# Performance work log

Hardware: AMD Instinct MI355X
Metric: run time of the kernel (lower is better)

## Reference

```python
import jax, jax.numpy as jnp
import numpy as np

EPS = 1e-5

def _ln(x, w, b):
    mu = jnp.mean(x, axis=-1, keepdims=True)
    var = jnp.var(x, axis=-1, keepdims=True)
    return (x - mu) * jax.lax.rsqrt(var + EPS) * w + b

def setup_inputs() -> dict:
    key = jax.random.key(0)
    ks = jax.random.split(key, 12)
    B, N, CZ, CH = 1, 384, 128, 128
    z = jax.random.normal(ks[0], (B, N, N, CZ), dtype=jnp.float32)
    mask = jnp.ones((B, N, N), dtype=jnp.float32)
    s_z = 1.0 / np.sqrt(CZ)
    s_h = 1.0 / np.sqrt(CH)
    return {
        "z": z,
        "mask": mask,
        "ln_in_w": jnp.ones((CZ,), jnp.float32),
        "ln_in_b": jnp.zeros((CZ,), jnp.float32),
        "w_a_g": jax.random.normal(ks[1], (CZ, CH), jnp.float32) * s_z,
        "b_a_g": jnp.ones((CH,), jnp.float32),
        "w_a_p": jax.random.normal(ks[2], (CZ, CH), jnp.float32) * s_z,
        "b_a_p": jnp.zeros((CH,), jnp.float32),
        "w_b_g": jax.random.normal(ks[3], (CZ, CH), jnp.float32) * s_z,
        "b_b_g": jnp.ones((CH,), jnp.float32),
        "w_b_p": jax.random.normal(ks[4], (CZ, CH), jnp.float32) * s_z,
        "b_b_p": jnp.zeros((CH,), jnp.float32),
        "ln_out_w": jnp.ones((CH,), jnp.float32),
        "ln_out_b": jnp.zeros((CH,), jnp.float32),
        "w_z": jax.random.normal(ks[5], (CH, CZ), jnp.float32) * s_h,
        "b_z": jnp.zeros((CZ,), jnp.float32),
        "w_g": jax.random.normal(ks[6], (CZ, CZ), jnp.float32) * s_z,
        "b_g": jnp.ones((CZ,), jnp.float32),
    }

def reference(z, mask, ln_in_w, ln_in_b, w_a_g, b_a_g, w_a_p, b_a_p,
              w_b_g, b_b_g, w_b_p, b_b_p, ln_out_w, ln_out_b,
              w_z, b_z, w_g, b_g):
    m = mask[..., None]                                   # [B,N,N,1]
    zn = _ln(z, ln_in_w, ln_in_b)                         # [B,N,N,Cz]
    a = m * jax.nn.sigmoid(zn @ w_a_g + b_a_g) * (zn @ w_a_p + b_a_p)
    b = m * jax.nn.sigmoid(zn @ w_b_g + b_b_g) * (zn @ w_b_p + b_b_p)
    # outgoing: p[b,i,j,c] = sum_k a[b,i,k,c] * b[b,j,k,c]
    x = jnp.einsum('bikc,bjkc->bijc', a, b)
    x = _ln(x, ln_out_w, ln_out_b)
    x = (x @ w_z + b_z) * jax.nn.sigmoid(zn @ w_g + b_g)
    return x
```

## Files before the change

kernel.cpp:

```cpp
#include <hip/hip_runtime.h>
#include <hip/hip_bf16.h>

#define NN 384
#define NP (NN*NN)
#define CC 128

typedef __attribute__((ext_vector_type(8))) short bf16x8;
typedef __attribute__((ext_vector_type(4))) float f32x4;
typedef __attribute__((ext_vector_type(8))) unsigned short u16x8;
typedef __attribute__((ext_vector_type(4))) unsigned short u16x4;

#define SW16(row, col) ((col) ^ (((row)&15)<<3))
#define SW8(row, col)  ((col) ^ (((row)&7)<<3))

__device__ __forceinline__ unsigned short f2bf(float f){
  unsigned int u = __float_as_uint(f);
  u += 0x7FFFu + ((u >> 16) & 1u);
  return (unsigned short)(u >> 16);
}
__device__ __forceinline__ float bf2f(unsigned short h){
  return __uint_as_float(((unsigned int)h) << 16);
}
__device__ __forceinline__ float sigm(float x){ return 1.f / (1.f + __expf(-x)); }

__global__ __launch_bounds__(256) void k0(const float* __restrict__ w0, const float* __restrict__ w1,
                                          const float* __restrict__ w2, const float* __restrict__ w3,
                                          const float* __restrict__ w4, const float* __restrict__ w5,
                                          unsigned short* __restrict__ Wt)
{
  __shared__ unsigned short t[CC*CC];
  const float* W = blockIdx.x==0?w0: blockIdx.x==1?w1: blockIdx.x==2?w2:
                   blockIdx.x==3?w3: blockIdx.x==4?w4: w5;
  unsigned short* o = Wt + blockIdx.x*CC*CC;
  for (int i = threadIdx.x; i < CC*CC; i += 256){
    int k = i >> 7, n = i & 127;
    t[n*CC + SW16(n, k)] = f2bf(W[i]);
  }
  __syncthreads();
  for (int i = threadIdx.x; i < CC*16; i += 256){
    int n = i >> 4, g = i & 15;
    *(u16x8*)&o[n*CC + g*8] = *(const u16x8*)&t[n*CC + SW16(n, g*8)];
  }
}

__global__ __launch_bounds__(256) void k1(
    const float* __restrict__ z, const float* __restrict__ mask,
    const float* __restrict__ lnw, const float* __restrict__ lnb,
    const float* __restrict__ bag, const float* __restrict__ bap,
    const float* __restrict__ bbg, const float* __restrict__ bbp,
    const float* __restrict__ bgt,
    const unsigned short* __restrict__ Wt,
    unsigned short* __restrict__ At, unsigned short* __restrict__ Bt,
    unsigned short* __restrict__ G)
{
  __shared__ unsigned short zn[CC*CC];
  const int tid = threadIdx.x, wave = tid>>6, lane = tid&63;
  const int l16 = lane&15, lg = lane>>4;
  const int posbase = blockIdx.x*128;

  {
    const int lh = lane&31, hh = lane>>5;
    const float4 lw4 = *(const float4*)&lnw[4*lh];
    const float4 lb4 = *(const float4*)&lnb[4*lh];
    for (int it = 0; it < 16; ++it){
      int pl = wave*32 + it*2 + hh;
      float4 v = *(const float4*)&z[(size_t)(posbase+pl)*CC + 4*lh];
      float s = v.x+v.y+v.z+v.w;
      float q = v.x*v.x+v.y*v.y+v.z*v.z+v.w*v.w;
      #pragma unroll
      for (int off = 16; off; off >>= 1){ s += __shfl_xor(s, off); q += __shfl_xor(q, off); }
      float mean = s*(1.f/128.f);
      float rstd = rsqrtf(q*(1.f/128.f) - mean*mean + 1e-5f);
      u16x4 o;
      o[0] = f2bf((v.x-mean)*rstd*lw4.x + lb4.x);
      o[1] = f2bf((v.y-mean)*rstd*lw4.y + lb4.y);
      o[2] = f2bf((v.z-mean)*rstd*lw4.z + lb4.z);
      o[3] = f2bf((v.w-mean)*rstd*lw4.w + lb4.w);
      *(u16x4*)&zn[pl*CC + SW16(pl, 4*lh)] = o;
    }
  }
  __syncthreads();

  #pragma unroll 1
  for (int pr = 0; pr < 2; ++pr){
    const unsigned short* Wg = Wt + (pr*2+0)*CC*CC;
    const unsigned short* Wp = Wt + (pr*2+1)*CC*CC;
    const float* Bg_ = pr ? bbg : bag;
    const float* Bp_ = pr ? bbp : bap;
    unsigned short* dst = pr ? Bt : At;
    float4 bg4[2], bp4[2];
    #pragma unroll
    for (int ma = 0; ma < 2; ++ma){
      int cb = wave*32 + ma*16 + lg*4;
      bg4[ma] = *(const float4*)&Bg_[cb];
      bp4[ma] = *(const float4*)&Bp_[cb];
    }
    #pragma unroll 1
    for (int half = 0; half < 2; ++half){
      f32x4 ag[2][4] = {}; f32x4 ap[2][4] = {};
      #pragma unroll
      for (int kc = 0; kc < 4; ++kc){
        const int kb = kc*32 + lg*8;
        bf16x8 bz[4], wgf[2], wpf[2];
        #pragma unroll
        for (int nb = 0; nb < 4; ++nb){
          int pos = half*64 + nb*16 + l16;
          bz[nb] = *(const bf16x8*)&zn[pos*CC + SW16(pos, kb)];
        }
        #pragma unroll
        for (int ma = 0; ma < 2; ++ma){
          int c = wave*32 + ma*16 + l16;
          wgf[ma] = *(const bf16x8*)&Wg[c*CC + kb];
          wpf[ma] = *(const bf16x8*)&Wp[c*CC + kb];
        }
        #pragma unroll
        for (int ma = 0; ma < 2; ++ma)
          #pragma unroll
          for (int nb = 0; nb < 4; ++nb){
            ag[ma][nb] = __builtin_amdgcn_mfma_f32_16x16x32_bf16(wgf[ma], bz[nb], ag[ma][nb], 0,0,0);
            ap[ma][nb] = __builtin_amdgcn_mfma_f32_16x16x32_bf16(wpf[ma], bz[nb], ap[ma][nb], 0,0,0);
          }
      }
      #pragma unroll
      for (int nb = 0; nb < 4; ++nb){
        int pos = posbase + half*64 + nb*16 + l16;
        float m = mask[pos];
        #pragma unroll
        for (int ma = 0; ma < 2; ++ma){
          int cb = wave*32 + ma*16 + lg*4;
          #pragma unroll
          for (int r = 0; r < 4; ++r){
            float bgv = r==0?bg4[ma].x : r==1?bg4[ma].y : r==2?bg4[ma].z : bg4[ma].w;
            float bpv = r==0?bp4[ma].x : r==1?bp4[ma].y : r==2?bp4[ma].z : bp4[ma].w;
            float v = m * sigm(ag[ma][nb][r] + bgv) * (ap[ma][nb][r] + bpv);
            dst[(size_t)(cb + r)*NP + pos] = f2bf(v);
          }
        }
      }
    }
  }

  {
    const unsigned short* Wgt = Wt + 4*CC*CC;
    f32x4 acc[2][8] = {};
    #pragma unroll
    for (int kc = 0; kc < 4; ++kc){
      const int kb = kc*32 + lg*8;
      bf16x8 az[2], wf[8];
      #pragma unroll
      for (int ma = 0; ma < 2; ++ma){
        int pos = wave*32 + ma*16 + l16;
        az[ma] = *(const bf16x8*)&zn[pos*CC + SW16(pos, kb)];
      }
      #pragma unroll
      for (int nr = 0; nr < 8; ++nr)
        wf[nr] = *(const bf16x8*)&Wgt[(nr*16+l16)*CC + kb];
      #pragma unroll
      for (int ma = 0; ma < 2; ++ma)
        #pragma unroll
        for (int nr = 0; nr < 8; ++nr)
          acc[ma][nr] = __builtin_amdgcn_mfma_f32_16x16x32_bf16(az[ma], wf[nr], acc[ma][nr], 0,0,0);
    }
    #pragma unroll
    for (int nr = 0; nr < 8; ++nr){
      int c = nr*16 + l16;
      float bv = bgt[c];
      #pragma unroll
      for (int ma = 0; ma < 2; ++ma)
        #pragma unroll
        for (int r = 0; r < 4; ++r){
          int pos = posbase + wave*32 + ma*16 + lg*4 + r;
          G[(size_t)pos*CC + c] = f2bf(sigm(acc[ma][nr][r] + bv));
        }
    }
  }
}

__global__ __launch_bounds__(256) void k2(const unsigned short* __restrict__ At,
                                          const unsigned short* __restrict__ Bt,
                                          unsigned short* __restrict__ Xt)
{
  __shared__ unsigned short As[128*64];
  __shared__ unsigned short Bs[128*64];
  const int c  = blockIdx.y;
  const int ti = blockIdx.x / 3, tj = blockIdx.x % 3;
  const int tid = threadIdx.x, wave = tid >> 6, lane = tid & 63;
  const int l16 = lane & 15, lg = lane >> 4;
  const unsigned short* Ag = At + (size_t)c*NP + (size_t)(ti*128)*NN;
  const unsigned short* Bg = Bt + (size_t)c*NP + (size_t)(tj*128)*NN;
  f32x4 acc[2][8] = {};
  for (int k0 = 0; k0 < NN; k0 += 64){
    __syncthreads();
    #pragma unroll
    for (int it = 0; it < 4; ++it){
      int i = tid + it*256;
      int row = i >> 3, g = i & 7;
      u16x8 va = *(const u16x8*)&Ag[(size_t)row*NN + k0 + g*8];
      u16x8 vb = *(const u16x8*)&Bg[(size_t)row*NN + k0 + g*8];
      *(u16x8*)&As[row*64 + SW8(row, g*8)] = va;
      *(u16x8*)&Bs[row*64 + SW8(row, g*8)] = vb;
    }
    __syncthreads();
    #pragma unroll
    for (int kc = 0; kc < 2; ++kc){
      const int kb = kc*32 + lg*8;
      bf16x8 af[2], bfr[8];
      #pragma unroll
      for (int ma = 0; ma < 2; ++ma){
        int row = wave*32 + ma*16 + l16;
        af[ma] = *(const bf16x8*)&As[row*64 + SW8(row, kb)];
      }
      #pragma unroll
      for (int nr = 0; nr < 8; ++nr){
        int row = nr*16 + l16;
        bfr[nr] = *(const bf16x8*)&Bs[row*64 + SW8(row, kb)];
      }
      #pragma unroll
      for (int ma = 0; ma < 2; ++ma)
        #pragma unroll
        for (int nr = 0; nr < 8; ++nr)
          acc[ma][nr] = __builtin_amdgcn_mfma_f32_16x16x32_bf16(af[ma], bfr[nr], acc[ma][nr], 0,0,0);
    }
  }
  size_t base = (size_t)c*NP + (size_t)(ti*128)*NN + tj*128;
  #pragma unroll
  for (int ma = 0; ma < 2; ++ma)
    #pragma unroll
    for (int nr = 0; nr < 8; ++nr)
      #pragma unroll
      for (int r = 0; r < 4; ++r){
        int row = wave*32 + ma*16 + lg*4 + r;
        int col = nr*16 + l16;
        Xt[base + (size_t)row*NN + col] = f2bf(acc[ma][nr][r]);
      }
}

__global__ __launch_bounds__(256) void k3(const unsigned short* __restrict__ Xt,
                                          const unsigned short* __restrict__ G,
                                          const float* __restrict__ lnw, const float* __restrict__ lnb,
                                          const unsigned short* __restrict__ Wzt, const float* __restrict__ bz,
                                          float* __restrict__ out)
{
  __shared__ unsigned short xc[CC*CC];
  __shared__ unsigned short yt[CC*CC];
  __shared__ float mu[CC], rs[CC];
  const int tid = threadIdx.x, wave = tid>>6, lane = tid&63;
  const int l16 = lane&15, lg = lane>>4;
  const int posbase = blockIdx.x*128;

  #pragma unroll
  for (int it = 0; it < 8; ++it){
    int i = tid + it*256;
    int cc = i >> 4, g = i & 15;
    u16x8 v = *(const u16x8*)&Xt[(size_t)cc*NP + posbase + g*8];
    *(u16x8*)&xc[cc*CC + SW16(cc, g*8)] = v;
  }
  __syncthreads();

  {
    const int lh = lane&31, hh = lane>>5;
    f32x4 s4 = {0,0,0,0}, q4 = {0,0,0,0};
    for (int ci = 0; ci < 64; ++ci){
      int cc = hh*64 + ci;
      u16x4 v = *(const u16x4*)&xc[cc*CC + SW16(cc, 4*lh)];
      #pragma unroll
      for (int j = 0; j < 4; ++j){
        float f = bf2f(v[j]);
        s4[j] += f; q4[j] += f*f;
      }
    }
    #pragma unroll
    for (int j = 0; j < 4; ++j){ s4[j] += __shfl_xor(s4[j], 32); q4[j] += __shfl_xor(q4[j], 32); }
    if (hh == 0){
      f32x4 m4, r4;
      #pragma unroll
      for (int j = 0; j < 4; ++j){
        float mean = s4[j]*(1.f/128.f);
        m4[j] = mean;
        r4[j] = rsqrtf(q4[j]*(1.f/128.f) - mean*mean + 1e-5f);
      }
      *(f32x4*)&mu[4*lh] = m4;
      *(f32x4*)&rs[4*lh] = r4;
    }
  }
  __syncthreads();

  #pragma unroll
  for (int it = 0; it < 8; ++it){
    int i = tid + it*256;
    int cc = i & 127, g = i >> 7;
    u16x8 v = *(const u16x8*)&xc[cc*CC + SW16(cc, g*8)];
    float lw = lnw[cc], lb = lnb[cc];
    #pragma unroll
    for (int j = 0; j < 8; ++j){
      int pos = g*8 + j;
      float f = (bf2f(v[j]) - mu[pos]) * rs[pos] * lw + lb;
      yt[pos*CC + SW16(pos, cc)] = f2bf(f);
    }
  }
  __syncthreads();

  f32x4 acc[2][8] = {};
  #pragma unroll
  for (int kc = 0; kc < 4; ++kc){
    const int kb = kc*32 + lg*8;
    bf16x8 af[2], wf[8];
    #pragma unroll
    for (int ma = 0; ma < 2; ++ma){
      int pos = wave*32 + ma*16 + l16;
      af[ma] = *(const bf16x8*)&yt[pos*CC + SW16(pos, kb)];
    }
    #pragma unroll
    for (int nr = 0; nr < 8; ++nr)
      wf[nr] = *(const bf16x8*)&Wzt[(nr*16+l16)*CC + kb];
    #pragma unroll
    for (int ma = 0; ma < 2; ++ma)
      #pragma unroll
      for (int nr = 0; nr < 8; ++nr)
        acc[ma][nr] = __builtin_amdgcn_mfma_f32_16x16x32_bf16(af[ma], wf[nr], acc[ma][nr], 0,0,0);
  }
  #pragma unroll
  for (int nr = 0; nr < 8; ++nr){
    int cch = nr*16 + l16;
    float bzv = bz[cch];
    #pragma unroll
    for (int ma = 0; ma < 2; ++ma)
      #pragma unroll
      for (int r = 0; r < 4; ++r){
        int pos = posbase + wave*32 + ma*16 + lg*4 + r;
        size_t o = (size_t)pos*CC + cch;
        out[o] = (acc[ma][nr][r] + bzv) * bf2f(G[o]);
      }
  }
}

extern "C" void kernel_launch(void* const* d_in, const int* in_sizes, int n_in,
                              void* d_out, int out_size, void* d_ws, size_t ws_size,
                              hipStream_t stream)
{
  const float* z    = (const float*)d_in[0];
  const float* mask = (const float*)d_in[1];
  const float* lniw = (const float*)d_in[2];
  const float* lnib = (const float*)d_in[3];
  const float* wag  = (const float*)d_in[4];
  const float* bag  = (const float*)d_in[5];
  const float* wap  = (const float*)d_in[6];
  const float* bap  = (const float*)d_in[7];
  const float* wbg  = (const float*)d_in[8];
  const float* bbg  = (const float*)d_in[9];
  const float* wbp  = (const float*)d_in[10];
  const float* bbp  = (const float*)d_in[11];
  const float* lnow = (const float*)d_in[12];
  const float* lnob = (const float*)d_in[13];
  const float* wz   = (const float*)d_in[14];
  const float* bz   = (const float*)d_in[15];
  const float* wg   = (const float*)d_in[16];
  const float* bg   = (const float*)d_in[17];
  float* out = (float*)d_out;

  unsigned short* Wt = (unsigned short*)d_ws;
  unsigned short* At = Wt + 6*CC*CC;
  unsigned short* Bt = At + (size_t)CC*NP;
  unsigned short* G  = Bt + (size_t)CC*NP;
  unsigned short* Xt = G  + (size_t)CC*NP;

  k0<<<6, 256, 0, stream>>>(wag, wap, wbg, wbp, wg, wz, Wt);
  k1<<<NP/128, 256, 0, stream>>>(z, mask, lniw, lnib, bag, bap, bbg, bbp, bg, Wt, At, Bt, G);
  k2<<<dim3(9, CC), 256, 0, stream>>>(At, Bt, Xt);
  k3<<<NP/128, 256, 0, stream>>>(Xt, G, lnow, lnob, Wt + 5*CC*CC, bz, out);
}
```

Before: 400.7 us.

## Split input projection kernel and fold output LayerNorm into projection epilogue

Splits the fused input-LN plus projection kernel into an LN kernel that writes normalized bf16 z to workspace and a projection kernel gridded over 64-row tiles and three projection types (a, b, gate). The tiles are loaded into LDS via global_load_lds. This gives more parallel blocks and lower register and LDS pressure, at the cost of an extra round trip of normalized z through global memory. The output LayerNorm is folded algebraically: the weight is pre-scaled by ln_out_w, and a per-channel weight sum and adjusted bias are precomputed. The projection therefore consumes the raw x tile, applied as rstd*acc - rstd*mean*wsum + b', which removes the normalized intermediate buffer and a pass in k3. Reading A fragments as transposed scalar LDS loads may add LDS instruction cost.

```diff
diff --git a/kernel.cpp b/kernel.cpp
--- a/kernel.cpp
+++ b/kernel.cpp
@@ -13,6 +13,12 @@
 #define SW16(row, col) ((col) ^ (((row)&15)<<3))
 #define SW8(row, col)  ((col) ^ (((row)&7)<<3))
 
+typedef const __attribute__((address_space(1))) unsigned int GLu32;
+typedef __attribute__((address_space(3))) unsigned int LDu32;
+__device__ __forceinline__ void gload_lds16(const void* g, void* l){
+  __builtin_amdgcn_global_load_lds((GLu32*)g, (LDu32*)l, 16, 0, 0);
+}
+
 __device__ __forceinline__ unsigned short f2bf(float f){
   unsigned int u = __float_as_uint(f);
   u += 0x7FFFu + ((u >> 16) & 1u);
@@ -26,15 +32,37 @@
 __global__ __launch_bounds__(256) void k0(const float* __restrict__ w0, const float* __restrict__ w1,
                                           const float* __restrict__ w2, const float* __restrict__ w3,
                                           const float* __restrict__ w4, const float* __restrict__ w5,
-                                          unsigned short* __restrict__ Wt)
-{
+                                          const float* __restrict__ lnow, const float* __restrict__ lnob,
+                                          const float* __restrict__ bz,
+                                          unsigned short* __restrict__ Wt,
+                                          float* __restrict__ wsum, float* __restrict__ bzp)
+{
+  if (blockIdx.x == 6){
+    __shared__ float p1[256], p2[256];
+    int c = threadIdx.x & 127, half = threadIdx.x >> 7;
+    float s1 = 0.f, s2 = 0.f;
+    #pragma unroll 8
+    for (int k = half*64; k < half*64 + 64; ++k){
+      float w = w5[k*CC + c];
+      s1 += lnow[k]*w; s2 += lnob[k]*w;
+    }
+    p1[threadIdx.x] = s1; p2[threadIdx.x] = s2;
+    __syncthreads();
+    if (half == 0){
+      wsum[c] = s1 + p1[128 + c];
+      bzp[c]  = bz[c] + s2 + p2[128 + c];
+    }
+    return;
+  }
   __shared__ unsigned short t[CC*CC];
   const float* W = blockIdx.x==0?w0: blockIdx.x==1?w1: blockIdx.x==2?w2:
                    blockIdx.x==3?w3: blockIdx.x==4?w4: w5;
+  const bool scale = (blockIdx.x == 5);
   unsigned short* o = Wt + blockIdx.x*CC*CC;
   for (int i = threadIdx.x; i < CC*CC; i += 256){
     int k = i >> 7, n = i & 127;
-    t[n*CC + SW16(n, k)] = f2bf(W[i]);
+    float f = W[i] * (scale ? lnow[k] : 1.0f);
+    t[n*CC + SW16(n, k)] = f2bf(f);
   }
   __syncthreads();
   for (int i = threadIdx.x; i < CC*16; i += 256){
@@ -43,135 +71,133 @@
   }
 }
 
-__global__ __launch_bounds__(256) void k1(
-    const float* __restrict__ z, const float* __restrict__ mask,
+__global__ __launch_bounds__(256) void k1a(const float* __restrict__ z,
     const float* __restrict__ lnw, const float* __restrict__ lnb,
+    unsigned short* __restrict__ zng)
+{
+  const int wave = threadIdx.x>>6, lane = threadIdx.x&63;
+  const int lh = lane&31, hh = lane>>5;
+  const float4 lw4 = *(const float4*)&lnw[4*lh];
+  const float4 lb4 = *(const float4*)&lnb[4*lh];
+  const int rowbase = blockIdx.x*128 + wave*32;
+  for (int it = 0; it < 16; ++it){
+    int pos = rowbase + it*2 + hh;
+    float4 v = *(const float4*)&z[(size_t)pos*CC + 4*lh];
+    float s = v.x+v.y+v.z+v.w;
+    float q = v.x*v.x+v.y*v.y+v.z*v.z+v.w*v.w;
+    #pragma unroll
+    for (int off = 16; off; off >>= 1){ s += __shfl_xor(s, off); q += __shfl_xor(q, off); }
+    float mean = s*(1.f/128.f);
+    float rstd = rsqrtf(q*(1.f/128.f) - mean*mean + 1e-5f);
+    u16x4 o;
+    o[0] = f2bf((v.x-mean)*rstd*lw4.x + lb4.x);
+    o[1] = f2bf((v.y-mean)*rstd*lw4.y + lb4.y);
+    o[2] = f2bf((v.z-mean)*rstd*lw4.z + lb4.z);
+    o[3] = f2bf((v.w-mean)*rstd*lw4.w + lb4.w);
+    *(u16x4*)&zng[(size_t)pos*CC + ((4*lh) ^ ((pos&15)<<3))] = o;
+  }
+}
+
+__global__ __launch_bounds__(256,3) void k1b(
+    const unsigned short* __restrict__ zng, const float* __restrict__ mask,
     const float* __restrict__ bag, const float* __restrict__ bap,
     const float* __restrict__ bbg, const float* __restrict__ bbp,
-    const float* __restrict__ bgt,
-    const unsigned short* __restrict__ Wt,
+    const float* __restrict__ bgt, const unsigned short* __restrict__ Wt,
     unsigned short* __restrict__ At, unsigned short* __restrict__ Bt,
     unsigned short* __restrict__ G)
 {
-  __shared__ unsigned short zn[CC*CC];
+  __shared__ unsigned short zn[64*CC];
   const int tid = threadIdx.x, wave = tid>>6, lane = tid&63;
   const int l16 = lane&15, lg = lane>>4;
-  const int posbase = blockIdx.x*128;
+  const int type = blockIdx.y;
+  const int tb = blockIdx.x*64;
 
   {
-    const int lh = lane&31, hh = lane>>5;
-    const float4 lw4 = *(const float4*)&lnw[4*lh];
-    const float4 lb4 = *(const float4*)&lnb[4*lh];
-    for (int it = 0; it < 16; ++it){
-      int pl = wave*32 + it*2 + hh;
-      float4 v = *(const float4*)&z[(size_t)(posbase+pl)*CC + 4*lh];
-      float s = v.x+v.y+v.z+v.w;
-      float q = v.x*v.x+v.y*v.y+v.z*v.z+v.w*v.w;
-      #pragma unroll
-      for (int off = 16; off; off >>= 1){ s += __shfl_xor(s, off); q += __shfl_xor(q, off); }
-      float mean = s*(1.f/128.f);
-      float rstd = rsqrtf(q*(1.f/128.f) - mean*mean + 1e-5f);
-      u16x4 o;
-      o[0] = f2bf((v.x-mean)*rstd*lw4.x + lb4.x);
-      o[1] = f2bf((v.y-mean)*rstd*lw4.y + lb4.y);
-      o[2] = f2bf((v.z-mean)*rstd*lw4.z + lb4.z);
-      o[3] = f2bf((v.w-mean)*rstd*lw4.w + lb4.w);
-      *(u16x4*)&zn[pl*CC + SW16(pl, 4*lh)] = o;
-    }
-  }
-  __syncthreads();
-
-  #pragma unroll 1
-  for (int pr = 0; pr < 2; ++pr){
-    const unsigned short* Wg = Wt + (pr*2+0)*CC*CC;
-    const unsigned short* Wp = Wt + (pr*2+1)*CC*CC;
-    const float* Bg_ = pr ? bbg : bag;
-    const float* Bp_ = pr ? bbp : bap;
-    unsigned short* dst = pr ? Bt : At;
-    float4 bg4[2], bp4[2];
+    const char* src = (const char*)(zng + (size_t)tb*CC);
+    #pragma unroll
+    for (int it = 0; it < 4; ++it){
+      int off = (wave*4 + it)*1024;
+      gload_lds16(src + off + lane*16, (char*)zn + off);
+    }
+  }
+  __syncthreads();
+
+  if (type < 2){
+    const unsigned short* Wg = Wt + (type*2+0)*CC*CC;
+    const unsigned short* Wp = Wt + (type*2+1)*CC*CC;
+    f32x4 ag[2][4] = {}, ap[2][4] = {};
+    #pragma unroll
+    for (int kc = 0; kc < 4; ++kc){
+      const int kb = kc*32 + lg*8;
+      bf16x8 bz[4], wgf[2], wpf[2];
+      #pragma unroll
+      for (int nb = 0; nb < 4; ++nb){
+        int pl = nb*16 + l16;
+        bz[nb] = *(const bf16x8*)&zn[pl*CC + (kb ^ (l16<<3))];
+      }
+      #pragma unroll
+      for (int ma = 0; ma < 2; ++ma){
+        int c = wave*32 + ma*16 + l16;
+        wgf[ma] = *(const bf16x8*)&Wg[c*CC + kb];
+        wpf[ma] = *(const bf16x8*)&Wp[c*CC + kb];
+      }
+      #pragma unroll
+      for (int ma = 0; ma < 2; ++ma)
+        #pragma unroll
+        for (int nb = 0; nb < 4; ++nb){
+          ag[ma][nb] = __builtin_amdgcn_mfma_f32_16x16x32_bf16(wgf[ma], bz[nb], ag[ma][nb], 0,0,0);
+          ap[ma][nb] = __builtin_amdgcn_mfma_f32_16x16x32_bf16(wpf[ma], bz[nb], ap[ma][nb], 0,0,0);
+        }
+    }
+    const float* Bg_ = type ? bbg : bag;
+    const float* Bp_ = type ? bbp : bap;
+    unsigned short* dst = type ? Bt : At;
+    f32x4 bg4[2], bp4[2];
     #pragma unroll
     for (int ma = 0; ma < 2; ++ma){
       int cb = wave*32 + ma*16 + lg*4;
-      bg4[ma] = *(const float4*)&Bg_[cb];
-      bp4[ma] = *(const float4*)&Bp_[cb];
-    }
-    #pragma unroll 1
-    for (int half = 0; half < 2; ++half){
-      f32x4 ag[2][4] = {}; f32x4 ap[2][4] = {};
-      #pragma unroll
-      for (int kc = 0; kc < 4; ++kc){
-        const int kb = kc*32 + lg*8;
-        bf16x8 bz[4], wgf[2], wpf[2];
+      bg4[ma] = *(const f32x4*)&Bg_[cb];
+      bp4[ma] = *(const f32x4*)&Bp_[cb];
+    }
+    #pragma unroll
+    for (int nb = 0; nb < 4; ++nb){
+      int pos = tb + nb*16 + l16;
+      float m = mask[pos];
+      #pragma unroll
+      for (int ma = 0; ma < 2; ++ma){
+        int cb = wave*32 + ma*16 + lg*4;
         #pragma unroll
-        for (int nb = 0; nb < 4; ++nb){
-          int pos = half*64 + nb*16 + l16;
-          bz[nb] = *(const bf16x8*)&zn[pos*CC + SW16(pos, kb)];
+        for (int r = 0; r < 4; ++r){
+          float v = m * sigm(ag[ma][nb][r] + bg4[ma][r]) * (ap[ma][nb][r] + bp4[ma][r]);
+          dst[(size_t)(cb + r)*NP + pos] = f2bf(v);
         }
-        #pragma unroll
-        for (int ma = 0; ma < 2; ++ma){
-          int c = wave*32 + ma*16 + l16;
-          wgf[ma] = *(const bf16x8*)&Wg[c*CC + kb];
-          wpf[ma] = *(const bf16x8*)&Wp[c*CC + kb];
-        }
-        #pragma unroll
-        for (int ma = 0; ma < 2; ++ma)
-          #pragma unroll
-          for (int nb = 0; nb < 4; ++nb){
-            ag[ma][nb] = __builtin_amdgcn_mfma_f32_16x16x32_bf16(wgf[ma], bz[nb], ag[ma][nb], 0,0,0);
-            ap[ma][nb] = __builtin_amdgcn_mfma_f32_16x16x32_bf16(wpf[ma], bz[nb], ap[ma][nb], 0,0,0);
-          }
-      }
-      #pragma unroll
-      for (int nb = 0; nb < 4; ++nb){
-        int pos = posbase + half*64 + nb*16 + l16;
-        float m = mask[pos];
-        #pragma unroll
-        for (int ma = 0; ma < 2; ++ma){
-          int cb = wave*32 + ma*16 + lg*4;
-          #pragma unroll
-          for (int r = 0; r < 4; ++r){
-            float bgv = r==0?bg4[ma].x : r==1?bg4[ma].y : r==2?bg4[ma].z : bg4[ma].w;
-            float bpv = r==0?bp4[ma].x : r==1?bp4[ma].y : r==2?bp4[ma].z : bp4[ma].w;
-            float v = m * sigm(ag[ma][nb][r] + bgv) * (ap[ma][nb][r] + bpv);
-            dst[(size_t)(cb + r)*NP + pos] = f2bf(v);
-          }
-        }
-      }
-    }
-  }
-
-  {
+      }
+    }
+  } else {
     const unsigned short* Wgt = Wt + 4*CC*CC;
-    f32x4 acc[2][8] = {};
+    f32x4 acc[8] = {};
     #pragma unroll
     for (int kc = 0; kc < 4; ++kc){
       const int kb = kc*32 + lg*8;
-      bf16x8 az[2], wf[8];
-      #pragma unroll
-      for (int ma = 0; ma < 2; ++ma){
-        int pos = wave*32 + ma*16 + l16;
-        az[ma] = *(const bf16x8*)&zn[pos*CC + SW16(pos, kb)];
-      }
+      int pl = wave*16 + l16;
+      bf16x8 az = *(const bf16x8*)&zn[pl*CC + (kb ^ (l16<<3))];
+      bf16x8 wf[8];
       #pragma unroll
       for (int nr = 0; nr < 8; ++nr)
         wf[nr] = *(const bf16x8*)&Wgt[(nr*16+l16)*CC + kb];
       #pragma unroll
-      for (int ma = 0; ma < 2; ++ma)
-        #pragma unroll
-        for (int nr = 0; nr < 8; ++nr)
-          acc[ma][nr] = __builtin_amdgcn_mfma_f32_16x16x32_bf16(az[ma], wf[nr], acc[ma][nr], 0,0,0);
+      for (int nr = 0; nr < 8; ++nr)
+        acc[nr] = __builtin_amdgcn_mfma_f32_16x16x32_bf16(az, wf[nr], acc[nr], 0,0,0);
     }
     #pragma unroll
     for (int nr = 0; nr < 8; ++nr){
       int c = nr*16 + l16;
       float bv = bgt[c];
       #pragma unroll
-      for (int ma = 0; ma < 2; ++ma)
-        #pragma unroll
-        for (int r = 0; r < 4; ++r){
-          int pos = posbase + wave*32 + ma*16 + lg*4 + r;
-          G[(size_t)pos*CC + c] = f2bf(sigm(acc[ma][nr][r] + bv));
-        }
+      for (int r = 0; r < 4; ++r){
+        int pos = tb + wave*16 + lg*4 + r;
+        G[(size_t)pos*CC + c] = f2bf(sigm(acc[nr][r] + bv));
+      }
     }
   }
 }
@@ -236,21 +262,20 @@
 }
 
 __global__ __launch_bounds__(256) void k3(const unsigned short* __restrict__ Xt,
-                                          const unsigned short* __restrict__ G,
-                                          const float* __restrict__ lnw, const float* __restrict__ lnb,
-                                          const unsigned short* __restrict__ Wzt, const float* __restrict__ bz,
-                                          float* __restrict__ out)
+    const unsigned short* __restrict__ G,
+    const unsigned short* __restrict__ Wzt, const float* __restrict__ wsum,
+    const float* __restrict__ bzp, float* __restrict__ out)
 {
   __shared__ unsigned short xc[CC*CC];
-  __shared__ unsigned short yt[CC*CC];
-  __shared__ float mu[CC], rs[CC];
+  __shared__ float sredS[8*CC], sredQ[8*CC];
+  __shared__ float rsl[CC], rml[CC];
   const int tid = threadIdx.x, wave = tid>>6, lane = tid&63;
   const int l16 = lane&15, lg = lane>>4;
   const int posbase = blockIdx.x*128;
 
   #pragma unroll
   for (int it = 0; it < 8; ++it){
-    int i = tid + it*256;
+    int i = it*256 + tid;
     int cc = i >> 4, g = i & 15;
     u16x8 v = *(const u16x8*)&Xt[(size_t)cc*NP + posbase + g*8];
     *(u16x8*)&xc[cc*CC + SW16(cc, g*8)] = v;
@@ -258,45 +283,27 @@
   __syncthreads();
 
   {
-    const int lh = lane&31, hh = lane>>5;
+    const int lh = tid & 31;
+    const int qq = tid >> 5;
     f32x4 s4 = {0,0,0,0}, q4 = {0,0,0,0};
-    for (int ci = 0; ci < 64; ++ci){
-      int cc = hh*64 + ci;
-      u16x4 v = *(const u16x4*)&xc[cc*CC + SW16(cc, 4*lh)];
-      #pragma unroll
-      for (int j = 0; j < 4; ++j){
-        float f = bf2f(v[j]);
-        s4[j] += f; q4[j] += f*f;
-      }
-    }
-    #pragma unroll
-    for (int j = 0; j < 4; ++j){ s4[j] += __shfl_xor(s4[j], 32); q4[j] += __shfl_xor(q4[j], 32); }
-    if (hh == 0){
-      f32x4 m4, r4;
-      #pragma unroll
-      for (int j = 0; j < 4; ++j){
-        float mean = s4[j]*(1.f/128.f);
-        m4[j] = mean;
-        r4[j] = rsqrtf(q4[j]*(1.f/128.f) - mean*mean + 1e-5f);
-      }
-      *(f32x4*)&mu[4*lh] = m4;
-      *(f32x4*)&rs[4*lh] = r4;
-    }
-  }
-  __syncthreads();
-
-  #pragma unroll
-  for (int it = 0; it < 8; ++it){
-    int i = tid + it*256;
-    int cc = i & 127, g = i >> 7;
-    u16x8 v = *(const u16x8*)&xc[cc*CC + SW16(cc, g*8)];
-    float lw = lnw[cc], lb = lnb[cc];
-    #pragma unroll
-    for (int j = 0; j < 8; ++j){
-      int pos = g*8 + j;
-      float f = (bf2f(v[j]) - mu[pos]) * rs[pos] * lw + lb;
-      yt[pos*CC + SW16(pos, cc)] = f2bf(f);
-    }
+    #pragma unroll
+    for (int ci = 0; ci < 16; ++ci){
+      int cc = qq*16 + ci;
+      u16x4 v = *(const u16x4*)&xc[cc*CC + ((4*lh) ^ ((cc&15)<<3))];
+      #pragma unroll
+      for (int j = 0; j < 4; ++j){ float f = bf2f(v[j]); s4[j] += f; q4[j] += f*f; }
+    }
+    *(f32x4*)&sredS[qq*CC + 4*lh] = s4;
+    *(f32x4*)&sredQ[qq*CC + 4*lh] = q4;
+  }
+  __syncthreads();
+  if (tid < 128){
+    float s = 0.f, q = 0.f;
+    #pragma unroll
+    for (int qq = 0; qq < 8; ++qq){ s += sredS[qq*CC + tid]; q += sredQ[qq*CC + tid]; }
+    float mean = s*(1.f/128.f);
+    float rstd = rsqrtf(q*(1.f/128.f) - mean*mean + 1e-5f);
+    rsl[tid] = rstd; rml[tid] = rstd*mean;
   }
   __syncthreads();
 
@@ -304,12 +311,19 @@
   #pragma unroll
   for (int kc = 0; kc < 4; ++kc){
     const int kb = kc*32 + lg*8;
-    bf16x8 af[2], wf[8];
+    bf16x8 af[2];
     #pragma unroll
     for (int ma = 0; ma < 2; ++ma){
       int pos = wave*32 + ma*16 + l16;
-      af[ma] = *(const bf16x8*)&yt[pos*CC + SW16(pos, kb)];
-    }
+      bf16x8 a;
+      #pragma unroll
+      for (int j = 0; j < 8; ++j){
+        int c = kb + j;
+        a[j] = (short)xc[c*CC + (pos ^ ((c&15)<<3))];
+      }
+      af[ma] = a;
+    }
+    bf16x8 wf[8];
     #pragma unroll
     for (int nr = 0; nr < 8; ++nr)
       wf[nr] = *(const bf16x8*)&Wzt[(nr*16+l16)*CC + kb];
@@ -319,17 +333,18 @@
       for (int nr = 0; nr < 8; ++nr)
         acc[ma][nr] = __builtin_amdgcn_mfma_f32_16x16x32_bf16(af[ma], wf[nr], acc[ma][nr], 0,0,0);
   }
+
   #pragma unroll
   for (int nr = 0; nr < 8; ++nr){
-    int cch = nr*16 + l16;
-    float bzv = bz[cch];
+    int c = nr*16 + l16;
+    float wsc = wsum[c], bzc = bzp[c];
     #pragma unroll
     for (int ma = 0; ma < 2; ++ma)
       #pragma unroll
       for (int r = 0; r < 4; ++r){
-        int pos = posbase + wave*32 + ma*16 + lg*4 + r;
-        size_t o = (size_t)pos*CC + cch;
-        out[o] = (acc[ma][nr][r] + bzv) * bf2f(G[o]);
+        int pl = wave*32 + ma*16 + lg*4 + r;
+        size_t o = (size_t)(posbase + pl)*CC + c;
+        out[o] = (rsl[pl]*acc[ma][nr][r] - rml[pl]*wsc + bzc) * bf2f(G[o]);
       }
   }
 }
@@ -359,13 +374,17 @@
   float* out = (float*)d_out;
 
   unsigned short* Wt = (unsigned short*)d_ws;
-  unsigned short* At = Wt + 6*CC*CC;
+  float* wsum = (float*)(Wt + 6*CC*CC);
+  float* bzp  = wsum + CC;
+  unsigned short* Xt = (unsigned short*)(bzp + CC + 64);
+  unsigned short* zng = Xt;
+  unsigned short* At = Xt + (size_t)CC*NP;
   unsigned short* Bt = At + (size_t)CC*NP;
   unsigned short* G  = Bt + (size_t)CC*NP;
-  unsigned short* Xt = G  + (size_t)CC*NP;
-
-  k0<<<6, 256, 0, stream>>>(wag, wap, wbg, wbp, wg, wz, Wt);
-  k1<<<NP/128, 256, 0, stream>>>(z, mask, lniw, lnib, bag, bap, bbg, bbp, bg, Wt, At, Bt, G);
+
+  k0<<<7, 256, 0, stream>>>(wag, wap, wbg, wbp, wg, wz, lnow, lnob, bz, Wt, wsum, bzp);
+  k1a<<<NP/128, 256, 0, stream>>>(z, lniw, lnib, zng);
+  k1b<<<dim3(NP/64, 3), 256, 0, stream>>>(zng, mask, bag, bap, bbg, bbp, bg, Wt, At, Bt, G);
   k2<<<dim3(9, CC), 256, 0, stream>>>(At, Bt, Xt);
-  k3<<<NP/128, 256, 0, stream>>>(Xt, G, lnow, lnob, Wt + 5*CC*CC, bz, out);
-}
+  k3<<<NP/128, 256, 0, stream>>>(Xt, G, Wt + 5*CC*CC, wsum, bzp, out);
+}
```

Result: no change. 393.9 us (-1.7%).
